# Kernel tuning notes

Hardware: AMD Instinct MI355X
Metric: run time of the kernel (lower is better)

The kernel has to match this reference:

```python
import jax, jax.numpy as jnp
import numpy as np

NB_COMP = 8
LAT_DIM = 512
NB_NEUR = 1024
OUT_DIM = 512
N_SAMPLES = 16384


def setup_inputs() -> dict:
    key = jax.random.key(0)
    ks = jax.random.split(key, 8)
    s1 = 1.0 / np.sqrt(LAT_DIM)
    s2 = 1.0 / np.sqrt(NB_NEUR)
    return {
        "epsilon": jax.random.normal(ks[0], (N_SAMPLES, LAT_DIM), dtype=jnp.float32),
        "comp_idx": jax.random.randint(ks[1], (N_SAMPLES,), 0, NB_COMP, dtype=jnp.int32),
        "mu": jnp.zeros((NB_COMP, LAT_DIM), dtype=jnp.float32),
        "rho": jnp.zeros((NB_COMP,), dtype=jnp.float32),  # sigma = softplus(rho)
        "W1": jax.random.normal(ks[2], (NB_COMP, LAT_DIM, NB_NEUR), dtype=jnp.float32) * s1,
        "b1": jax.random.normal(ks[3], (NB_COMP, NB_NEUR), dtype=jnp.float32) * s1,
        "W2": jax.random.normal(ks[4], (NB_COMP, NB_NEUR, OUT_DIM), dtype=jnp.float32) * s2,
        "b2": jax.random.normal(ks[5], (NB_COMP, OUT_DIM), dtype=jnp.float32) * s2,
    }


def reference(epsilon, comp_idx, mu, rho, W1, b1, W2, b2):
    # GNNens.forward: per-sample categorical component dispatch through a
    # 1-hidden-layer sigmoid MLP. Vectorized as compute-all-components + select.
    sigma = jax.nn.softplus(rho)                          # [C]
    # lat_c[c,n,d] = epsilon[n,d] * sigma[c] + mu[c,d]
    lat = epsilon[None, :, :] * sigma[:, None, None] + mu[:, None, :]  # [C,N,D]
    h = jax.nn.sigmoid(jnp.einsum('cnd,cdh->cnh', lat, W1) + b1[:, None, :])  # [C,N,H]
    y = jnp.einsum('cnh,cho->cno', h, W2) + b2[:, None, :]                    # [C,N,O]
    # select each sample's routed component
    idx = comp_idx[None, :, None].astype(jnp.int32)       # [1,N,1]
    out = jnp.take_along_axis(y, idx, axis=0)[0]          # [N,O]
    return out
```

## Files before the change

### kernel.cpp

```cpp
#include <hip/hip_runtime.h>
#include <stdint.h>

#define NCOMP 8
#define LATD  512
#define HID   1024
#define OUTD  512
#define NS    16384

typedef unsigned short u16;
typedef __bf16 bf16x8 __attribute__((ext_vector_type(8)));
typedef float  f32x4  __attribute__((ext_vector_type(4)));

#define MAPS       (NS/128 + NCOMP)
#define SLOT_CHUNK ((MAPS + 7)/8)

#define ORDER_OFF  2048
#define APACK_OFF  (ORDER_OFF + NS*4)
#define W1T_OFF    (APACK_OFF + (size_t)NS*LATD*2)
#define W2T_OFF    (W1T_OFF + (size_t)NCOMP*LATD*HID*2)
#define H_OFF      (W2T_OFF + (size_t)NCOMP*HID*OUTD*2)
#define WS_NEEDED  (H_OFF + (size_t)NS*HID*2)

__device__ __forceinline__ u16 f2b(float f) {
  unsigned int u = __builtin_bit_cast(unsigned int, f);
  u = (u + 0x7FFFu + ((u >> 16) & 1u)) >> 16;
  return (u16)u;
}

__device__ __forceinline__ void load_lds16(const void* g, void* l) {
  __builtin_amdgcn_global_load_lds((const __attribute__((address_space(1))) void*)g,
                                   (__attribute__((address_space(3))) void*)l, 16, 0, 0);
}

__global__ __launch_bounds__(1024)
void k_prep_all(const int* __restrict__ idx, const float* __restrict__ rho,
                const float* __restrict__ eps, const float* __restrict__ mu,
                const float* __restrict__ W1, const float* __restrict__ W2,
                int* __restrict__ offsets, int* __restrict__ ntiles,
                int* __restrict__ map, int* __restrict__ order,
                u16* __restrict__ Apack, u16* __restrict__ W1T, u16* __restrict__ W2T) {
  __shared__ float tile[64][65];
  __shared__ int hist_s[NCOMP];
  __shared__ int wtot[16];
  const int b = blockIdx.x;
  const int t = threadIdx.x;

  if (b < NCOMP) {
    const int c = b;
    const int wave = t >> 6, lane = t & 63;

    int my[16];
    #pragma unroll
    for (int i = 0; i < 16; ++i) my[i] = idx[t + (i << 10)];

    unsigned long long nib = 0;
    #pragma unroll
    for (int i = 0; i < 16; ++i) nib += 1ull << (my[i] << 2);

    if (t < NCOMP) hist_s[t] = 0;
    __syncthreads();

    #pragma unroll
    for (int cc = 0; cc < NCOMP; ++cc) {
      int v = (int)((nib >> (cc << 2)) & 15);
      #pragma unroll
      for (int d = 1; d < 64; d <<= 1) v += __shfl_xor(v, d);
      if (lane == 0) atomicAdd(&hist_s[cc], v);
    }

    int v = (int)((nib >> (c << 2)) & 15);
    int s = v;
    #pragma unroll
    for (int d = 1; d < 64; d <<= 1) {
      int u = __shfl_up(s, d);
      if (lane >= d) s += u;
    }
    if (lane == 63) wtot[wave] = s;
    __syncthreads();

    int wbase = 0;
    for (int w = 0; w < wave; ++w) wbase += wtot[w];
    int off_c = 0;
    #pragma unroll
    for (int cc = 0; cc < NCOMP; ++cc) if (cc < c) off_c += hist_s[cc];

    int pos = off_c + wbase + (s - v);
    #pragma unroll
    for (int i = 0; i < 16; ++i)
      if (my[i] == c) order[pos++] = t + (i << 10);

    if (t == 0) {
      if (c == 0) {
        int a = 0;
        for (int cc = 0; cc < NCOMP; ++cc) { offsets[cc] = a; a += hist_s[cc]; }
        offsets[NCOMP] = a;
        int tot = 0;
        for (int cc = 0; cc < NCOMP; ++cc) tot += (hist_s[cc] + 127) >> 7;
        ntiles[0] = tot;
      }
      int mb = 0;
      for (int cc = 0; cc < c; ++cc) mb += (hist_s[cc] + 127) >> 7;
      int nt = (hist_s[c] + 127) >> 7;
      for (int m = 0; m < nt; ++m) map[mb + m] = (c << 16) | m;
    }
  } else if (b < NCOMP + 1024) {
    int g = (b - NCOMP) * 1024 + t;
    int i = g >> 6;
    int d = (g & 63) << 3;
    int c = idx[i];
    float r = rho[c];
    float sg = (r > 20.f) ? r : log1pf(expf(r));
    const float4* ep = reinterpret_cast<const float4*>(eps + (size_t)i*LATD + d);
    const float4* mp = reinterpret_cast<const float4*>(mu  + (size_t)c*LATD + d);
    float4 e0 = ep[0], e1 = ep[1], m0 = mp[0], m1 = mp[1];
    unsigned o0 = f2b(e0.x*sg+m0.x), o1 = f2b(e0.y*sg+m0.y), o2 = f2b(e0.z*sg+m0.z), o3 = f2b(e0.w*sg+m0.w);
    unsigned o4 = f2b(e1.x*sg+m1.x), o5 = f2b(e1.y*sg+m1.y), o6 = f2b(e1.z*sg+m1.z), o7 = f2b(e1.w*sg+m1.w);
    uint4 pk;
    pk.x = o0 | (o1<<16); pk.y = o2 | (o3<<16); pk.z = o4 | (o5<<16); pk.w = o6 | (o7<<16);
    *reinterpret_cast<uint4*>(Apack + (size_t)i*LATD + d) = pk;
  } else {
    int bb = b - (NCOMP + 1024);
    const float* src; u16* dst; int CC, r0, c0;
    int R;
    if (bb < 1024) {
      int comp = bb >> 7, loc = bb & 127;
      R = LATD; CC = HID;
      c0 = (loc & 15) << 6; r0 = (loc >> 4) << 6;
      src = W1 + (size_t)comp*R*CC; dst = W1T + (size_t)comp*R*CC;
    } else {
      int b2 = bb - 1024;
      int comp = b2 >> 7, loc = b2 & 127;
      R = HID; CC = OUTD;
      c0 = (loc & 7) << 6; r0 = (loc >> 3) << 6;
      src = W2 + (size_t)comp*R*CC; dst = W2T + (size_t)comp*R*CC;
    }
    int tx = t & 63, ty = t >> 6;
    for (int rr = ty; rr < 64; rr += 16)
      tile[rr][tx] = src[(size_t)(r0+rr)*CC + c0 + tx];
    __syncthreads();
    for (int rr = ty; rr < 64; rr += 16)
      dst[(size_t)(c0+rr)*R + r0 + tx] = f2b(tile[tx][rr]);
  }
}

template<int K, int NB, int STAGE>
__global__ __launch_bounds__(256, 4)
void k_gemm(const u16* __restrict__ A, const u16* __restrict__ BT,
            const int* __restrict__ offsets, const int* __restrict__ ntiles,
            const int* __restrict__ map, const int* __restrict__ order,
            const float* __restrict__ bias,
            u16* __restrict__ Hout, float* __restrict__ Yout) {
  constexpr int NCB = NB/128;
  __shared__ u16 As[128*64];
  __shared__ u16 Bs[128*64];
  __shared__ int ord[128];

  const int id    = blockIdx.x;
  const int xcd   = id & 7;
  const int sub   = id >> 3;
  const int ncolb = sub % NCB;
  const int slot  = xcd*SLOT_CHUNK + sub / NCB;
  if (slot >= ntiles[0]) return;
  const int packed = map[slot];
  const int c      = packed >> 16;
  const int bstart = offsets[c];
  const int bend   = offsets[c+1];
  const int tile0  = bstart + (packed & 0xffff)*128;
  const int ncol0  = ncolb*128;

  const int tid  = threadIdx.x;
  const int wave = tid >> 6;
  const int lane = tid & 63;
  const int srow = (wave<<5) + (lane>>3);
  const int scol = ((lane & 7) ^ ((lane >> 3) & 7)) << 3;

  if (STAGE == 2 && tid < 128) {
    int gr = tile0 + tid;
    ord[tid] = order[gr < bend ? gr : bstart];
  }

  size_t a_off[4], b_off[4];
  const size_t bbase = (size_t)c * NB * K;
  #pragma unroll
  for (int i = 0; i < 4; ++i) {
    int ar = tile0 + srow + (i<<3);
    if (ar >= bend) ar = bend - 1;
    int arow = (STAGE == 1) ? order[ar] : ar;
    a_off[i] = (size_t)arow * K + scol;
    b_off[i] = bbase + (size_t)(ncol0 + srow + (i<<3)) * K + scol;
  }

  const int wr   = (wave >> 1) << 6;
  const int wc   = (wave & 1) << 6;
  const int quad = lane >> 4;
  const int l16  = lane & 15;
  const int sw   = l16 & 7;

  float bcol[4];
  #pragma unroll
  for (int ni = 0; ni < 4; ++ni)
    bcol[ni] = bias[(size_t)c*NB + ncol0 + wc + (ni<<4) + l16];

  f32x4 acc[4][4] = {};

  for (int k0 = 0; k0 < K; k0 += 64) {
    #pragma unroll
    for (int i = 0; i < 4; ++i)
      load_lds16(A + a_off[i] + k0, &As[((wave<<5) + (i<<3))<<6]);
    #pragma unroll
    for (int i = 0; i < 4; ++i)
      load_lds16(BT + b_off[i] + k0, &Bs[((wave<<5) + (i<<3))<<6]);
    __syncthreads();
    #pragma unroll
    for (int kk = 0; kk < 64; kk += 32) {
      const int kc = (kk >> 3) + quad;
      const int sc = (kc ^ sw) << 3;
      bf16x8 af[4], bfr[4];
      #pragma unroll
      for (int mi = 0; mi < 4; ++mi)
        af[mi] = *reinterpret_cast<const bf16x8*>(&As[((wr + (mi<<4) + l16)<<6) + sc]);
      #pragma unroll
      for (int ni = 0; ni < 4; ++ni)
        bfr[ni] = *reinterpret_cast<const bf16x8*>(&Bs[((wc + (ni<<4) + l16)<<6) + sc]);
      #pragma unroll
      for (int mi = 0; mi < 4; ++mi)
        #pragma unroll
        for (int ni = 0; ni < 4; ++ni)
          acc[mi][ni] = __builtin_amdgcn_mfma_f32_16x16x32_bf16(af[mi], bfr[ni], acc[mi][ni], 0, 0, 0);
    }
    __syncthreads();
  }

  #pragma unroll
  for (int mi = 0; mi < 4; ++mi) {
    #pragma unroll
    for (int r = 0; r < 4; ++r) {
      const int row_l = wr + (mi<<4) + (quad<<2) + r;
      const int grow  = tile0 + row_l;
      if (grow < bend) {
        #pragma unroll
        for (int ni = 0; ni < 4; ++ni) {
          const int col = ncol0 + wc + (ni<<4) + l16;
          float v = acc[mi][ni][r] + bcol[ni];
          if (STAGE == 1) {
            v = 1.0f / (1.0f + __expf(-v));
            Hout[(size_t)grow*NB + col] = f2b(v);
          } else {
            Yout[(size_t)ord[row_l]*NB + col] = v;
          }
        }
      }
    }
  }
}

__global__ void k_naive(const float* __restrict__ eps, const int* __restrict__ idx,
                        const float* __restrict__ mu, const float* __restrict__ rho,
                        const float* __restrict__ W1, const float* __restrict__ b1,
                        const float* __restrict__ W2, const float* __restrict__ b2,
                        float* __restrict__ out) {
  __shared__ float lat[LATD];
  __shared__ float h[HID];
  int n = blockIdx.x, t = threadIdx.x;
  int c = idx[n];
  float r = rho[c];
  float sg = (r > 20.f) ? r : log1pf(expf(r));
  for (int d = t; d < LATD; d += 256) lat[d] = eps[(size_t)n*LATD+d]*sg + mu[(size_t)c*LATD+d];
  __syncthreads();
  for (int j = t; j < HID; j += 256) {
    float a = b1[(size_t)c*HID+j];
    const float* w = W1 + (size_t)c*LATD*HID + j;
    for (int d = 0; d < LATD; ++d) a += lat[d]*w[(size_t)d*HID];
    h[j] = 1.f/(1.f+expf(-a));
  }
  __syncthreads();
  for (int o = t; o < OUTD; o += 256) {
    float a = b2[(size_t)c*OUTD+o];
    const float* w = W2 + (size_t)c*HID*OUTD + o;
    for (int j = 0; j < HID; ++j) a += h[j]*w[(size_t)j*OUTD];
    out[(size_t)n*OUTD+o] = a;
  }
}

extern "C" void kernel_launch(void* const* d_in, const int* in_sizes, int n_in,
                              void* d_out, int out_size, void* d_ws, size_t ws_size,
                              hipStream_t stream) {
  const float* eps = (const float*)d_in[0];
  const int*   idx = (const int*)d_in[1];
  const float* mu  = (const float*)d_in[2];
  const float* rho = (const float*)d_in[3];
  const float* W1  = (const float*)d_in[4];
  const float* b1  = (const float*)d_in[5];
  const float* W2  = (const float*)d_in[6];
  const float* b2  = (const float*)d_in[7];
  float* out = (float*)d_out;

  if (ws_size < WS_NEEDED) {
    k_naive<<<NS, 256, 0, stream>>>(eps, idx, mu, rho, W1, b1, W2, b2, out);
    return;
  }

  char* ws = (char*)d_ws;
  int*   offsets = (int*)(ws + 0);
  int*   ntiles  = (int*)(ws + 96);
  int*   map     = (int*)(ws + 128);
  int*   order   = (int*)(ws + ORDER_OFF);
  u16*   Apack   = (u16*)(ws + APACK_OFF);
  u16*   W1T     = (u16*)(ws + W1T_OFF);
  u16*   W2T     = (u16*)(ws + W2T_OFF);
  u16*   Hws     = (u16*)(ws + H_OFF);

  k_prep_all<<<NCOMP + 1024 + 2048, 1024, 0, stream>>>(
      idx, rho, eps, mu, W1, W2, offsets, ntiles, map, order, Apack, W1T, W2T);
  k_gemm<LATD, HID, 1><<<8*SLOT_CHUNK*(HID/128), 256, 0, stream>>>(
      Apack, W1T, offsets, ntiles, map, order, b1, Hws, nullptr);
  k_gemm<HID, OUTD, 2><<<8*SLOT_CHUNK*(OUTD/128), 256, 0, stream>>>(
      Hws, W2T, offsets, ntiles, map, order, b2, nullptr, out);
}
```

Baseline: 182.1 us.

## Enlarge GEMM M-tile to 256 rows with 8 waves and templated N-tile

The grouped GEMM kernels now use 256-row tiles with 512-thread blocks (8 waves), and the N-tile width is a template parameter: 128 for the first GEMM and 64 for the second. The routing map is rebuilt for 256-row tiles. Each B tile is meant to be reused across more rows, and the second GEMM gets more column blocks to keep parallelism up. The cost is more LDS per block, more padding waste per component, fewer blocks in the first GEMM, and possibly lower occupancy.

After: 193.5 us. +6.2%, slower.

```diff
diff --git a/kernel.cpp b/kernel.cpp
--- a/kernel.cpp
+++ b/kernel.cpp
@@ -11,7 +11,7 @@
 typedef __bf16 bf16x8 __attribute__((ext_vector_type(8)));
 typedef float  f32x4  __attribute__((ext_vector_type(4)));
 
-#define MAPS       (NS/128 + NCOMP)
+#define MAPS       (NS/256 + NCOMP)
 #define SLOT_CHUNK ((MAPS + 7)/8)
 
 #define ORDER_OFF  2048
@@ -95,12 +95,12 @@
         for (int cc = 0; cc < NCOMP; ++cc) { offsets[cc] = a; a += hist_s[cc]; }
         offsets[NCOMP] = a;
         int tot = 0;
-        for (int cc = 0; cc < NCOMP; ++cc) tot += (hist_s[cc] + 127) >> 7;
+        for (int cc = 0; cc < NCOMP; ++cc) tot += (hist_s[cc] + 255) >> 8;
         ntiles[0] = tot;
       }
       int mb = 0;
-      for (int cc = 0; cc < c; ++cc) mb += (hist_s[cc] + 127) >> 7;
-      int nt = (hist_s[c] + 127) >> 7;
+      for (int cc = 0; cc < c; ++cc) mb += (hist_s[cc] + 255) >> 8;
+      int nt = (hist_s[c] + 255) >> 8;
       for (int m = 0; m < nt; ++m) map[mb + m] = (c << 16) | m;
     }
   } else if (b < NCOMP + 1024) {
@@ -143,17 +143,19 @@
   }
 }
 
-template<int K, int NB, int STAGE>
-__global__ __launch_bounds__(256, 4)
+template<int K, int NB, int TN, int STAGE>
+__global__ __launch_bounds__(512, 4)
 void k_gemm(const u16* __restrict__ A, const u16* __restrict__ BT,
             const int* __restrict__ offsets, const int* __restrict__ ntiles,
             const int* __restrict__ map, const int* __restrict__ order,
             const float* __restrict__ bias,
             u16* __restrict__ Hout, float* __restrict__ Yout) {
-  constexpr int NCB = NB/128;
-  __shared__ u16 As[128*64];
-  __shared__ u16 Bs[128*64];
-  __shared__ int ord[128];
+  constexpr int NCB = NB/TN;
+  constexpr int FN  = TN/32;
+  constexpr int LB  = TN/64;
+  __shared__ u16 As[256*64];
+  __shared__ u16 Bs[TN*64];
+  __shared__ int ord[256];
 
   const int id    = blockIdx.x;
   const int xcd   = id & 7;
@@ -165,67 +167,68 @@
   const int c      = packed >> 16;
   const int bstart = offsets[c];
   const int bend   = offsets[c+1];
-  const int tile0  = bstart + (packed & 0xffff)*128;
-  const int ncol0  = ncolb*128;
+  const int tile0  = bstart + (packed & 0xffff)*256;
+  const int ncol0  = ncolb*TN;
 
   const int tid  = threadIdx.x;
   const int wave = tid >> 6;
   const int lane = tid & 63;
-  const int srow = (wave<<5) + (lane>>3);
   const int scol = ((lane & 7) ^ ((lane >> 3) & 7)) << 3;
 
-  if (STAGE == 2 && tid < 128) {
+  if (STAGE == 2 && tid < 256) {
     int gr = tile0 + tid;
     ord[tid] = order[gr < bend ? gr : bstart];
   }
 
-  size_t a_off[4], b_off[4];
+  size_t a_off[4], b_off[LB];
   const size_t bbase = (size_t)c * NB * K;
   #pragma unroll
   for (int i = 0; i < 4; ++i) {
-    int ar = tile0 + srow + (i<<3);
+    int ar = tile0 + (wave<<5) + (i<<3) + (lane>>3);
     if (ar >= bend) ar = bend - 1;
     int arow = (STAGE == 1) ? order[ar] : ar;
     a_off[i] = (size_t)arow * K + scol;
-    b_off[i] = bbase + (size_t)(ncol0 + srow + (i<<3)) * K + scol;
-  }
+  }
+  #pragma unroll
+  for (int i = 0; i < LB; ++i)
+    b_off[i] = bbase + (size_t)(ncol0 + wave*(TN/8) + (i<<3) + (lane>>3)) * K + scol;
 
   const int wr   = (wave >> 1) << 6;
-  const int wc   = (wave & 1) << 6;
+  const int wc   = (wave & 1) * (TN/2);
   const int quad = lane >> 4;
   const int l16  = lane & 15;
   const int sw   = l16 & 7;
 
-  float bcol[4];
+  float bcol[FN];
   #pragma unroll
-  for (int ni = 0; ni < 4; ++ni)
+  for (int ni = 0; ni < FN; ++ni)
     bcol[ni] = bias[(size_t)c*NB + ncol0 + wc + (ni<<4) + l16];
 
-  f32x4 acc[4][4] = {};
+  f32x4 acc[4][FN] = {};
 
   for (int k0 = 0; k0 < K; k0 += 64) {
     #pragma unroll
     for (int i = 0; i < 4; ++i)
       load_lds16(A + a_off[i] + k0, &As[((wave<<5) + (i<<3))<<6]);
     #pragma unroll
-    for (int i = 0; i < 4; ++i)
-      load_lds16(BT + b_off[i] + k0, &Bs[((wave<<5) + (i<<3))<<6]);
+    for (int i = 0; i < LB; ++i)
+      load_lds16(BT + b_off[i] + k0, &Bs[(wave*(TN/8) + (i<<3))<<6]);
     __syncthreads();
     #pragma unroll
     for (int kk = 0; kk < 64; kk += 32) {
       const int kc = (kk >> 3) + quad;
       const int sc = (kc ^ sw) << 3;
-      bf16x8 af[4], bfr[4];
+      bf16x8 af[4], bfr[FN];
       #pragma unroll
       for (int mi = 0; mi < 4; ++mi)
         af[mi] = *reinterpret_cast<const bf16x8*>(&As[((wr + (mi<<4) + l16)<<6) + sc]);
       #pragma unroll
-      for (int ni = 0; ni < 4; ++ni)
+      for (int ni = 0; ni < FN; ++ni)
         bfr[ni] = *reinterpret_cast<const bf16x8*>(&Bs[((wc + (ni<<4) + l16)<<6) + sc]);
       #pragma unroll
       for (int mi = 0; mi < 4; ++mi)
         #pragma unroll
-        for (int ni = 0; ni < 4; ++ni)
+        for (int ni = 0; ni < FN; ++ni)
           acc[mi][ni] = __builtin_amdgcn_mfma_f32_16x16x32_bf16(af[mi], bfr[ni], acc[mi][ni], 0, 0, 0);
     }
     __syncthreads();
@@ -239,7 +242,7 @@
       const int grow  = tile0 + row_l;
       if (grow < bend) {
         #pragma unroll
-        for (int ni = 0; ni < 4; ++ni) {
+        for (int ni = 0; ni < FN; ++ni) {
           const int col = ncol0 + wc + (ni<<4) + l16;
           float v = acc[mi][ni][r] + bcol[ni];
           if (STAGE == 1) {
@@ -312,8 +315,8 @@
 
   k_prep_all<<<NCOMP + 1024 + 2048, 1024, 0, stream>>>(
       idx, rho, eps, mu, W1, W2, offsets, ntiles, map, order, Apack, W1T, W2T);
-  k_gemm<LATD, HID, 1><<<8*SLOT_CHUNK*(HID/128), 256, 0, stream>>>(
+  k_gemm<LATD, HID, 128, 1><<<8*SLOT_CHUNK*(HID/128), 512, 0, stream>>>(
       Apack, W1T, offsets, ntiles, map, order, b1, Hws, nullptr);
-  k_gemm<HID, OUTD, 2><<<8*SLOT_CHUNK*(OUTD/128), 256, 0, stream>>>(
+  k_gemm<HID, OUTD, 64, 2><<<8*SLOT_CHUNK*(OUTD/64), 512, 0, stream>>>(
       Hws, W2T, offsets, ntiles, map, order, b2, nullptr, out);
 }
```
